# Kernel tuning notes

Hardware: AMD Instinct MI355X
Metric: run time of the kernel (lower is better)

The kernel has to match this reference:

```python
import jax, jax.numpy as jnp
import numpy as np

EPS = 1e-6

def _rms_norm(x, w):
    # per-head RMSNorm over last dim (head_dim)
    var = jnp.mean(jnp.square(x), axis=-1, keepdims=True)
    return x * jax.lax.rsqrt(var + EPS) * w

def _linear(x, w, b):
    # torch nn.Linear: y = x @ W^T + b
    return jnp.einsum('bsd,od->bso', x, w) + b

def setup_inputs() -> dict:
    key = jax.random.key(0)
    ks = jax.random.split(key, 16)
    B, S, S_enc, D, H, HD = 1, 2048, 256, 1536, 24, 64
    w = lambda k: jax.random.normal(k, (D, D), dtype=jnp.float32) * 0.02
    return {
        'hidden_states': jax.random.normal(ks[0], (B, S, D), dtype=jnp.float32),
        'encoder_hidden_states': jax.random.normal(ks[1], (B, S_enc, D), dtype=jnp.float32),
        'attention_mask': jnp.zeros((B, 1, 1, S + S_enc), dtype=jnp.float32),
        'to_q_weight': w(ks[2]), 'to_q_bias': jnp.zeros((D,), jnp.float32),
        'to_k_weight': w(ks[3]), 'to_k_bias': jnp.zeros((D,), jnp.float32),
        'to_v_weight': w(ks[4]), 'to_v_bias': jnp.zeros((D,), jnp.float32),
        'norm_q_weight': jnp.ones((HD,), jnp.float32),
        'norm_k_weight': jnp.ones((HD,), jnp.float32),
        'add_q_proj_weight': w(ks[5]), 'add_q_proj_bias': jnp.zeros((D,), jnp.float32),
        'add_k_proj_weight': w(ks[6]), 'add_k_proj_bias': jnp.zeros((D,), jnp.float32),
        'add_v_proj_weight': w(ks[7]), 'add_v_proj_bias': jnp.zeros((D,), jnp.float32),
        'norm_added_q_weight': jnp.ones((HD,), jnp.float32),
        'norm_added_k_weight': jnp.ones((HD,), jnp.float32),
        'to_out_0_weight': w(ks[8]), 'to_out_0_bias': jnp.zeros((D,), jnp.float32),
        'to_add_out_weight': w(ks[9]), 'to_add_out_bias': jnp.zeros((D,), jnp.float32),
        'attn_heads': 24,
        'attn_head_dim': 64,
    }

def reference(hidden_states, encoder_hidden_states, attention_mask,
              to_q_weight, to_q_bias, to_k_weight, to_k_bias, to_v_weight, to_v_bias,
              norm_q_weight, norm_k_weight,
              add_q_proj_weight, add_q_proj_bias, add_k_proj_weight, add_k_proj_bias,
              add_v_proj_weight, add_v_proj_bias,
              norm_added_q_weight, norm_added_k_weight,
              to_out_0_weight, to_out_0_bias, to_add_out_weight, to_add_out_bias,
              attn_heads, attn_head_dim):
    B, S, D = hidden_states.shape
    S_enc = encoder_hidden_states.shape[1]
    H, HD = attn_heads, attn_head_dim
    scale = float(HD) ** -0.5

    def split_heads(x):  # [B,T,H*HD] -> [B,H,T,HD]
        return x.reshape(B, -1, H, HD).transpose(0, 2, 1, 3)

    # hidden-stream QKV + per-head RMSNorm on q,k
    q = _rms_norm(split_heads(_linear(hidden_states, to_q_weight, to_q_bias)), norm_q_weight)
    k = _rms_norm(split_heads(_linear(hidden_states, to_k_weight, to_k_bias)), norm_k_weight)
    v = split_heads(_linear(hidden_states, to_v_weight, to_v_bias))

    # encoder-stream QKV + per-head RMSNorm on q,k
    eq = _rms_norm(split_heads(_linear(encoder_hidden_states, add_q_proj_weight, add_q_proj_bias)), norm_added_q_weight)
    ek = _rms_norm(split_heads(_linear(encoder_hidden_states, add_k_proj_weight, add_k_proj_bias)), norm_added_k_weight)
    ev = split_heads(_linear(encoder_hidden_states, add_v_proj_weight, add_v_proj_bias))

    # concat streams along sequence: [B,H,S+S_enc,HD]
    q = jnp.concatenate([q, eq], axis=2)
    k = jnp.concatenate([k, ek], axis=2)
    v = jnp.concatenate([v, ev], axis=2)

    # SDPA with additive mask
    scores = jnp.einsum('bhqd,bhkd->bhqk', q, k) * scale + attention_mask
    probs = jax.nn.softmax(scores, axis=-1)
    out = jnp.einsum('bhqk,bhkd->bhqd', probs, v)  # [B,H,T,HD]
    out = out.transpose(0, 2, 1, 3).reshape(B, S + S_enc, H * HD)

    # split back into image / text streams, separate output projections
    attn_output = _linear(out[:, :S], to_out_0_weight, to_out_0_bias)
    context_attn_output = _linear(out[:, S:], to_add_out_weight, to_add_out_bias)
    del context_attn_output  # AttentionFunc returns only the hidden-stream output
    return attn_output
```

## Files before the change

### kernel.cpp

```cpp
#include <hip/hip_runtime.h>
#include <cstdint>


typedef __attribute__((ext_vector_type(8))) short s16x8;
typedef __attribute__((ext_vector_type(4))) float f32x4;

#define LOG2E 1.4426950408889634f

__device__ __forceinline__ short f2bf(float f) {
  union { float f; uint32_t u; } v; v.f = f;
  uint32_t r = v.u + 0x7FFFu + ((v.u >> 16) & 1u);
  return (short)(r >> 16);
}

__device__ __forceinline__ uint32_t cvt_pk_bf16(float lo, float hi) {
  uint32_t r;
  asm("v_cvt_pk_bf16_f32 %0, %1, %2" : "=v"(r) : "v"(lo), "v"(hi));
  return r;
}

typedef uint32_t __attribute__((address_space(1)))* gas_u32;
typedef uint32_t __attribute__((address_space(3)))* las_u32;

__device__ __forceinline__ void gload_lds16(const short* g, short* l) {
  __builtin_amdgcn_global_load_lds((gas_u32)(g), (las_u32)(l), 16, 0, 0);
}

struct CvtSeg { const float* src; short* dst; int n4; };
struct CvtArgs { CvtSeg s[8]; const float* msrc; float* mdst; int mn4; };

__global__ __launch_bounds__(256) void cvt_bf16_kernel(CvtArgs a) {
  const int stride = gridDim.x * blockDim.x;
  const int tid = blockIdx.x * blockDim.x + threadIdx.x;
  for (int i = 0; i < 8; ++i) {
    const float4* src = (const float4*)a.s[i].src;
    short* dst = a.s[i].dst;
    const int n4 = a.s[i].n4;
    for (int j = tid; j < n4; j += stride) {
      float4 v = src[j];
      short4 o;
      o.x = f2bf(v.x); o.y = f2bf(v.y); o.z = f2bf(v.z); o.w = f2bf(v.w);
      *(short4*)(dst + (size_t)j * 4) = o;
    }
  }
  const float4* ms = (const float4*)a.msrc;
  float4* md = (float4*)a.mdst;
  for (int j = tid; j < a.mn4; j += stride) {
    float4 m = ms[j];
    float4 o = {m.x * LOG2E, m.y * LOG2E, m.z * LOG2E, m.w * LOG2E};
    md[j] = o;
  }
}

enum { MODE_Q = 0, MODE_K = 1, MODE_V = 2, MODE_OUT = 3 };

struct GemmCfg {
  const short* A;
  const short* W;
  const float* bias;
  const float* normw;
  void* dst;
  int toff;
  int mode;
  int pad;
};
struct GemmArgs { GemmCfg c[5]; };

__global__ __launch_bounds__(256) void proj_gemm_kernel(GemmArgs args, int chunk) {
  const int w = (blockIdx.x & 7) * chunk + (blockIdx.x >> 3);
  int z, tx, ty;
  if (w < 576) { z = w / 192; const int r = w % 192; tx = r >> 4; ty = r & 15; }
  else { int r = w - 576; z = 3 + r / 24; r %= 24; tx = r >> 1; ty = r & 1; }
  const GemmCfg cfg = args.c[z];
  constexpr int K = 1536;
  __shared__ short As[4096];
  __shared__ short Bs[4096];
  const int t = threadIdx.x;
  const int lane = t & 63;
  const int wave = t >> 6;
  const int l16 = lane & 15;
  const int quad = lane >> 4;
  const int wm = wave >> 1;
  const int wn = wave & 1;

  const short* __restrict__ Ag = cfg.A + (size_t)(ty * 128) * K;
  const short* __restrict__ Wg = cfg.W + (size_t)(tx * 128) * K;
  const int srow = t >> 2;
  const int ssw = ((t & 3) ^ ((srow >> 1) & 3)) << 3;
  const int rsw = (quad ^ ((l16 >> 1) & 3)) << 3;

  const f32x4 z4 = {0.f, 0.f, 0.f, 0.f};
  f32x4 acc[4][4];
#pragma unroll
  for (int i = 0; i < 4; ++i) {
#pragma unroll
    for (int j = 0; j < 4; ++j) acc[i][j] = z4;
  }

  for (int k0 = 0; k0 < K; k0 += 32) {
    gload_lds16(Ag + (size_t)srow * K + k0 + ssw, As + t * 8);
    gload_lds16(Ag + (size_t)(srow + 64) * K + k0 + ssw, As + 2048 + t * 8);
    gload_lds16(Wg + (size_t)srow * K + k0 + ssw, Bs + t * 8);
    gload_lds16(Wg + (size_t)(srow + 64) * K + k0 + ssw, Bs + 2048 + t * 8);
    __syncthreads();
    s16x8 af[4], bfr[4];
#pragma unroll
    for (int i = 0; i < 4; ++i)
      af[i] = *(const s16x8*)(As + (wm * 64 + i * 16 + l16) * 32 + rsw);
#pragma unroll
    for (int i = 0; i < 4; ++i)
      bfr[i] = *(const s16x8*)(Bs + (wn * 64 + i * 16 + l16) * 32 + rsw);
#pragma unroll
    for (int mi = 0; mi < 4; ++mi) {
#pragma unroll
      for (int ni = 0; ni < 4; ++ni)
        acc[mi][ni] = __builtin_amdgcn_mfma_f32_16x16x32_bf16(af[mi], bfr[ni], acc[mi][ni], 0, 0, 0);
    }
    __syncthreads();
  }

  const int nbase = tx * 128 + wn * 64;
  const int mbase = ty * 128 + wm * 64;
  const int mode = cfg.mode;
  const int h = nbase >> 6;

  float biasv[4], nwv[4];
#pragma unroll
  for (int ni = 0; ni < 4; ++ni) {
    int col = nbase + ni * 16 + l16;
    biasv[ni] = cfg.bias[col];
    nwv[ni] = (mode == MODE_Q || mode == MODE_K) ? cfg.normw[col & 63] : 0.f;
  }

#pragma unroll
  for (int mi = 0; mi < 4; ++mi) {
    float vv[4][4];
#pragma unroll
    for (int ni = 0; ni < 4; ++ni) {
#pragma unroll
      for (int r = 0; r < 4; ++r) vv[ni][r] = acc[mi][ni][r] + biasv[ni];
    }
    if (mode == MODE_Q || mode == MODE_K) {
      float ss[4];
#pragma unroll
      for (int r = 0; r < 4; ++r)
        ss[r] = vv[0][r] * vv[0][r] + vv[1][r] * vv[1][r] +
                vv[2][r] * vv[2][r] + vv[3][r] * vv[3][r];
#pragma unroll
      for (int r = 0; r < 4; ++r) {
        ss[r] += __shfl_xor(ss[r], 1);
        ss[r] += __shfl_xor(ss[r], 2);
        ss[r] += __shfl_xor(ss[r], 4);
        ss[r] += __shfl_xor(ss[r], 8);
        float rs = rsqrtf(ss[r] * (1.0f / 64.0f) + 1e-6f);
#pragma unroll
        for (int ni = 0; ni < 4; ++ni) vv[ni][r] *= rs * nwv[ni];
      }
    }
    const int row0 = mbase + mi * 16 + quad * 4;
    if (mode == MODE_Q) {
      short* Qd = (short*)cfg.dst;
#pragma unroll
      for (int ni = 0; ni < 4; ++ni) {
        int d = ni * 16 + l16;
#pragma unroll
        for (int r = 0; r < 4; ++r)
          Qd[((size_t)h * 2048 + row0 + r) * 64 + d] = f2bf(vv[ni][r]);
      }
    } else if (mode == MODE_K) {
      short* Kd = (short*)cfg.dst;
#pragma unroll
      for (int ni = 0; ni < 4; ++ni) {
        int d = ni * 16 + l16;
#pragma unroll
        for (int r = 0; r < 4; ++r)
          Kd[((size_t)h * 2304 + cfg.toff + row0 + r) * 64 + d] = f2bf(vv[ni][r]);
      }
    } else if (mode == MODE_V) {
      short* Vd = (short*)cfg.dst;
#pragma unroll
      for (int ni = 0; ni < 4; ++ni) {
        int d = ni * 16 + l16;
        short4 o4;
        o4.x = f2bf(vv[ni][0]); o4.y = f2bf(vv[ni][1]);
        o4.z = f2bf(vv[ni][2]); o4.w = f2bf(vv[ni][3]);
        *(short4*)(Vd + ((size_t)h * 64 + d) * 2304 + cfg.toff + row0) = o4;
      }
    } else {
      float* Od = (float*)cfg.dst;
#pragma unroll
      for (int ni = 0; ni < 4; ++ni) {
        int col = nbase + ni * 16 + l16;
#pragma unroll
        for (int r = 0; r < 4; ++r)
          Od[(size_t)(row0 + r) * 1536 + col] = vv[ni][r];
      }
    }
  }
}

__global__ __launch_bounds__(256) void flash_kernel(
    const short* __restrict__ Q, const short* __restrict__ Kc,
    const short* __restrict__ VT, const float* __restrict__ mlt,
    short* __restrict__ AO) {
  const int b = blockIdx.x;
  const int h = (b & 7) * 3 + ((b >> 3) % 3);
  const int q0 = ((b >> 3) / 3) * 64;
  const int lane = threadIdx.x & 63;
  const int wave = threadIdx.x >> 6;
  const int qw = wave & 1;
  const int ks = wave >> 1;
  const int l16 = lane & 15;
  const int quad = lane >> 4;

  __shared__ __align__(16) short smem[16384];

  const short* Kh = Kc + (size_t)h * 2304 * 64;
  const short* Vh = VT + (size_t)h * 64 * 2304;

  s16x8 aq0[2], aq1[2];
#pragma unroll
  for (int g = 0; g < 2; ++g) {
    const short* Qrow =
        Q + ((size_t)h * 2048 + q0 + qw * 32 + g * 16 + l16) * 64;
    aq0[g] = *(const s16x8*)(Qrow + quad * 8);
    aq1[g] = *(const s16x8*)(Qrow + quad * 8 + 32);
  }

  s16x8 ones;
#pragma unroll
  for (int i = 0; i < 8; ++i) ones[i] = (short)0x3F80;

  const f32x4 z4 = {0.f, 0.f, 0.f, 0.f};
  f32x4 o[2][4];
#pragma unroll
  for (int g = 0; g < 2; ++g)
#pragma unroll
    for (int mi = 0; mi < 4; ++mi) o[g][mi] = z4;
  f32x4 lacc[2] = {z4, z4};
  const float SC = 0.125f * LOG2E;
  const int kbase = ks * 1152;

  const int gi0 = qw * 64 + lane;
  const int trow0 = gi0 >> 3, cp0 = gi0 & 7;
  const int srow0 = ((trow0 & 12) << 1) | (trow0 & 3);
  const int d0 = gi0 >> 2, cpv0 = gi0 & 3;
  const short* kS = Kh + (size_t)kbase * 64 + srow0 * 64 + ((cp0 ^ (trow0 & 7)) << 3);
  const short* vS = Vh + (size_t)d0 * 2304 + kbase + ((cpv0 ^ ((d0 >> 1) & 3)) << 3);
  const int ldst = qw * 512 + lane * 8;

  auto stage = [&](int it, int buf) {
    short* kt = smem + (ks * 2 + buf) * 2048;
    short* vt = smem + 8192 + (ks * 2 + buf) * 2048;
    const short* ksrc = kS + it * 2048;
    const short* vsrc = vS + it * 32;
    gload_lds16(ksrc,             kt + ldst);
    gload_lds16(ksrc + 256,       kt + 1024 + ldst);
    gload_lds16(vsrc,             vt + ldst);
    gload_lds16(vsrc + 32 * 2304, vt + 1024 + ldst);
  };

  stage(0, 0);
  __syncthreads();

#pragma unroll 2
  for (int it = 0; it < 36; ++it) {
    const int buf = it & 1;
    if (it < 35) stage(it + 1, buf ^ 1);
    const short* kt = smem + (ks * 2 + buf) * 2048;
    const short* vt = smem + 8192 + (ks * 2 + buf) * 2048;
    const int kb = kbase + it * 32;

    s16x8 bk[2][2];
#pragma unroll
    for (int ni = 0; ni < 2; ++ni) {
      const int tt = ni * 16 + l16;
      const short* kr = kt + tt * 64;
      bk[ni][0] = *(const s16x8*)(kr + ((quad ^ (tt & 7)) << 3));
      bk[ni][1] = *(const s16x8*)(kr + (((quad + 4) ^ (tt & 7)) << 3));
    }
    s16x8 bv[4];
#pragma unroll
    for (int mi = 0; mi < 4; ++mi) {
      const int d = mi * 16 + l16;
      bv[mi] = *(const s16x8*)(vt + d * 32 + ((quad ^ ((d >> 1) & 3)) << 3));
    }
    float4 mv0 = *(const float4*)(mlt + kb + quad * 8);
    float4 mv1 = *(const float4*)(mlt + kb + quad * 8 + 4);
    const float m8[8] = {mv0.x, mv0.y, mv0.z, mv0.w, mv1.x, mv1.y, mv1.z, mv1.w};

#pragma unroll
    for (int g = 0; g < 2; ++g) {
      union { uint32_t w[4]; s16x8 v; } pu;
#pragma unroll
      for (int ni = 0; ni < 2; ++ni) {
        f32x4 s = __builtin_amdgcn_mfma_f32_16x16x32_bf16(bk[ni][0], aq0[g], z4, 0, 0, 0);
        s = __builtin_amdgcn_mfma_f32_16x16x32_bf16(bk[ni][1], aq1[g], s, 0, 0, 0);
        float p[4];
#pragma unroll
        for (int rr = 0; rr < 4; ++rr)
          p[rr] = __builtin_amdgcn_exp2f(fmaf(s[rr], SC, m8[ni * 4 + rr]));
        pu.w[ni * 2 + 0] = cvt_pk_bf16(p[0], p[1]);
        pu.w[ni * 2 + 1] = cvt_pk_bf16(p[2], p[3]);
      }
      lacc[g] = __builtin_amdgcn_mfma_f32_16x16x32_bf16(pu.v, ones, lacc[g], 0, 0, 0);
#pragma unroll
      for (int mi = 0; mi < 4; ++mi)
        o[g][mi] = __builtin_amdgcn_mfma_f32_16x16x32_bf16(pu.v, bv[mi], o[g][mi], 0, 0, 0);
    }
    __syncthreads();
  }

  f32x4* R = (f32x4*)smem;
  if (ks == 1) {
    f32x4* Rw = R + (qw * 64 + lane) * 10;
#pragma unroll
    for (int g = 0; g < 2; ++g) {
#pragma unroll
      for (int mi = 0; mi < 4; ++mi) Rw[g * 5 + mi] = o[g][mi];
      Rw[g * 5 + 4] = lacc[g];
    }
  }
  __syncthreads();
  if (ks == 0) {
    const f32x4* Rw = R + (qw * 64 + lane) * 10;
#pragma unroll
    for (int g = 0; g < 2; ++g) {
#pragma unroll
      for (int mi = 0; mi < 4; ++mi) o[g][mi] += Rw[g * 5 + mi];
      f32x4 lt = lacc[g] + Rw[g * 5 + 4];
#pragma unroll
      for (int rr = 0; rr < 4; ++rr) {
        float inv = 1.0f / lt[rr];
        int tq = q0 + qw * 32 + g * 16 + quad * 4 + rr;
#pragma unroll
        for (int mi = 0; mi < 4; ++mi)
          AO[(size_t)tq * 1536 + h * 64 + mi * 16 + l16] = f2bf(o[g][mi][rr] * inv);
      }
    }
  }
}

extern "C" void kernel_launch(void* const* d_in, const int* in_sizes, int n_in,
                              void* d_out, int out_size, void* d_ws, size_t ws_size,
                              hipStream_t stream) {
  (void)in_sizes; (void)n_in; (void)out_size; (void)ws_size;
  const float* hidden = (const float*)d_in[0];
  const float* enc    = (const float*)d_in[1];
  const float* amask  = (const float*)d_in[2];
  const float* wq  = (const float*)d_in[3];  const float* bq  = (const float*)d_in[4];
  const float* wk  = (const float*)d_in[5];  const float* bk  = (const float*)d_in[6];
  const float* wv  = (const float*)d_in[7];  const float* bv  = (const float*)d_in[8];
  const float* nqw = (const float*)d_in[9];  const float* nkw = (const float*)d_in[10];
  const float* wak = (const float*)d_in[13]; const float* bak = (const float*)d_in[14];
  const float* wav = (const float*)d_in[15]; const float* bav = (const float*)d_in[16];
  const float* nakw = (const float*)d_in[18];
  const float* wo  = (const float*)d_in[19]; const float* bo  = (const float*)d_in[20];
  float* out = (float*)d_out;

  char* p = (char*)d_ws;
  auto carve = [&](size_t bytes) { char* r = p; p += (bytes + 255) & ~(size_t)255; return r; };
  short* Xb   = (short*)carve((size_t)2048 * 1536 * 2);
  short* Eb   = (short*)carve((size_t)256 * 1536 * 2);
  short* Wqb  = (short*)carve((size_t)1536 * 1536 * 2);
  short* Wkb  = (short*)carve((size_t)1536 * 1536 * 2);
  short* Wvb  = (short*)carve((size_t)1536 * 1536 * 2);
  short* Wakb = (short*)carve((size_t)1536 * 1536 * 2);
  short* Wavb = (short*)carve((size_t)1536 * 1536 * 2);
  short* Wob  = (short*)carve((size_t)1536 * 1536 * 2);
  short* Qb   = (short*)carve((size_t)24 * 2048 * 64 * 2);
  short* Kb   = (short*)carve((size_t)24 * 2304 * 64 * 2);
  short* VTb  = (short*)carve((size_t)24 * 64 * 2304 * 2);
  short* AOb  = (short*)carve((size_t)2048 * 1536 * 2);
  float* MLb  = (float*)carve((size_t)2304 * 4);

  CvtArgs ca;
  ca.s[0] = {hidden, Xb, 2048 * 1536 / 4};
  ca.s[1] = {enc,    Eb, 256 * 1536 / 4};
  ca.s[2] = {wq,  Wqb,  1536 * 1536 / 4};
  ca.s[3] = {wk,  Wkb,  1536 * 1536 / 4};
  ca.s[4] = {wv,  Wvb,  1536 * 1536 / 4};
  ca.s[5] = {wak, Wakb, 1536 * 1536 / 4};
  ca.s[6] = {wav, Wavb, 1536 * 1536 / 4};
  ca.s[7] = {wo,  Wob,  1536 * 1536 / 4};
  ca.msrc = amask; ca.mdst = MLb; ca.mn4 = 2304 / 4;
  cvt_bf16_kernel<<<dim3(1024), dim3(256), 0, stream>>>(ca);

  GemmArgs g1;
  g1.c[0] = {Xb, Wqb,  bq,  nqw,     (void*)Qb,  0,    MODE_Q, 0};
  g1.c[1] = {Xb, Wkb,  bk,  nkw,     (void*)Kb,  0,    MODE_K, 0};
  g1.c[2] = {Xb, Wvb,  bv,  nullptr, (void*)VTb, 0,    MODE_V, 0};
  g1.c[3] = {Eb, Wakb, bak, nakw,    (void*)Kb,  2048, MODE_K, 0};
  g1.c[4] = {Eb, Wavb, bav, nullptr, (void*)VTb, 2048, MODE_V, 0};
  proj_gemm_kernel<<<dim3(624), dim3(256), 0, stream>>>(g1, 78);

  flash_kernel<<<dim3(768), dim3(256), 0, stream>>>(Qb, Kb, VTb, MLb, AOb);

  GemmArgs g3;
  g3.c[0] = {AOb, Wob, bo, nullptr, (void*)out, 0, MODE_OUT, 0};
  proj_gemm_kernel<<<dim3(192), dim3(256), 0, stream>>>(g3, 24);
}
```

Baseline: 273.5 us.

## Fuse Q/K/V projections into one GEMM kernel sharing the activation tile

Adds a dedicated QKV GEMM kernel where each block loads one 128-row activation tile once and multiplies it against the Q, K and V weight tiles (64 columns each) at the same time, keeping three accumulator sets. The encoder stream does the same with its K and V weights. This cuts activation reloads and the block count from 624 to 432. In exchange each block uses more registers and LDS, which may lower occupancy, and 432 blocks may fill the GPU's compute units less evenly.

Result: no change. 278.9 us (+2.0%).

```diff
diff --git a/kernel.cpp b/kernel.cpp
--- a/kernel.cpp
+++ b/kernel.cpp
@@ -65,6 +65,145 @@
   int pad;
 };
 struct GemmArgs { GemmCfg c[5]; };
+
+__global__ __launch_bounds__(256) void qkv_gemm_kernel(GemmArgs args) {
+  const int w = (blockIdx.x & 7) * 54 + (blockIdx.x >> 3);
+  int zc, tx, ty;
+  GemmCfg s0, s1, s2;
+  if (w < 384) {
+    zc = 3; tx = w >> 4; ty = w & 15;
+    s0 = args.c[0]; s1 = args.c[1]; s2 = args.c[2];
+  } else {
+    const int r = w - 384;
+    zc = 2; tx = r >> 1; ty = r & 1;
+    s0 = args.c[3]; s1 = args.c[4]; s2 = args.c[4];
+  }
+  constexpr int K = 1536;
+  __shared__ short As[4096];
+  __shared__ short Ws[3][2048];
+  const int t = threadIdx.x;
+  const int lane = t & 63;
+  const int wave = t >> 6;
+  const int l16 = lane & 15;
+  const int quad = lane >> 4;
+
+  const short* __restrict__ Ag = s0.A + (size_t)(ty * 128) * K;
+  const short* __restrict__ W0 = s0.W + (size_t)(tx * 64) * K;
+  const short* __restrict__ W1 = s1.W + (size_t)(tx * 64) * K;
+  const short* __restrict__ W2 = s2.W + (size_t)(tx * 64) * K;
+  const int srow = t >> 2;
+  const int ssw = ((t & 3) ^ ((srow >> 1) & 3)) << 3;
+  const int rsw = (quad ^ ((l16 >> 1) & 3)) << 3;
+
+  const f32x4 z4 = {0.f, 0.f, 0.f, 0.f};
+  f32x4 acc[3][2][4];
+#pragma unroll
+  for (int z = 0; z < 3; ++z)
+#pragma unroll
+    for (int i = 0; i < 2; ++i)
+#pragma unroll
+      for (int j = 0; j < 4; ++j) acc[z][i][j] = z4;
+
+  for (int k0 = 0; k0 < K; k0 += 32) {
+    gload_lds16(Ag + (size_t)srow * K + k0 + ssw, As + t * 8);
+    gload_lds16(Ag + (size_t)(srow + 64) * K + k0 + ssw, As + 2048 + t * 8);
+    gload_lds16(W0 + (size_t)srow * K + k0 + ssw, Ws[0] + t * 8);
+    gload_lds16(W1 + (size_t)srow * K + k0 + ssw, Ws[1] + t * 8);
+    if (zc == 3) gload_lds16(W2 + (size_t)srow * K + k0 + ssw, Ws[2] + t * 8);
+    __syncthreads();
+    s16x8 af[2];
+    af[0] = *(const s16x8*)(As + (wave * 32 + l16) * 32 + rsw);
+    af[1] = *(const s16x8*)(As + (wave * 32 + 16 + l16) * 32 + rsw);
+#pragma unroll
+    for (int z = 0; z < 3; ++z) {
+      if (z < zc) {
+        s16x8 bfr[4];
+#pragma unroll
+        for (int i = 0; i < 4; ++i)
+          bfr[i] = *(const s16x8*)(Ws[z] + (i * 16 + l16) * 32 + rsw);
+#pragma unroll
+        for (int mi = 0; mi < 2; ++mi)
+#pragma unroll
+          for (int ni = 0; ni < 4; ++ni)
+            acc[z][mi][ni] = __builtin_amdgcn_mfma_f32_16x16x32_bf16(
+                af[mi], bfr[ni], acc[z][mi][ni], 0, 0, 0);
+      }
+    }
+    __syncthreads();
+  }
+
+  const int h = tx;
+  const int nbase = tx * 64;
+#pragma unroll
+  for (int z = 0; z < 3; ++z) {
+    if (z >= zc) continue;
+    const GemmCfg cfg = (z == 0) ? s0 : (z == 1) ? s1 : s2;
+    const int mode = cfg.mode;
+    float biasv[4], nwv[4];
+#pragma unroll
+    for (int ni = 0; ni < 4; ++ni) {
+      int col = nbase + ni * 16 + l16;
+      biasv[ni] = cfg.bias[col];
+      nwv[ni] = (mode == MODE_Q || mode == MODE_K) ? cfg.normw[col & 63] : 0.f;
+    }
+#pragma unroll
+    for (int mi = 0; mi < 2; ++mi) {
+      float vv[4][4];
+#pragma unroll
+      for (int ni = 0; ni < 4; ++ni) {
+#pragma unroll
+        for (int r = 0; r < 4; ++r) vv[ni][r] = acc[z][mi][ni][r] + biasv[ni];
+      }
+      if (mode == MODE_Q || mode == MODE_K) {
+        float ss[4];
+#pragma unroll
+        for (int r = 0; r < 4; ++r)
+          ss[r] = vv[0][r] * vv[0][r] + vv[1][r] * vv[1][r] +
+                  vv[2][r] * vv[2][r] + vv[3][r] * vv[3][r];
+#pragma unroll
+        for (int r = 0; r < 4; ++r) {
+          ss[r] += __shfl_xor(ss[r], 1);
+          ss[r] += __shfl_xor(ss[r], 2);
+          ss[r] += __shfl_xor(ss[r], 4);
+          ss[r] += __shfl_xor(ss[r], 8);
+          float rs = rsqrtf(ss[r] * (1.0f / 64.0f) + 1e-6f);
+#pragma unroll
+          for (int ni = 0; ni < 4; ++ni) vv[ni][r] *= rs * nwv[ni];
+        }
+      }
+      const int row0 = ty * 128 + wave * 32 + mi * 16 + quad * 4;
+      if (mode == MODE_Q) {
+        short* Qd = (short*)cfg.dst;
+#pragma unroll
+        for (int ni = 0; ni < 4; ++ni) {
+          int d = ni * 16 + l16;
+#pragma unroll
+          for (int r = 0; r < 4; ++r)
+            Qd[((size_t)h * 2048 + row0 + r) * 64 + d] = f2bf(vv[ni][r]);
+        }
+      } else if (mode == MODE_K) {
+        short* Kd = (short*)cfg.dst;
+#pragma unroll
+        for (int ni = 0; ni < 4; ++ni) {
+          int d = ni * 16 + l16;
+#pragma unroll
+          for (int r = 0; r < 4; ++r)
+            Kd[((size_t)h * 2304 + cfg.toff + row0 + r) * 64 + d] = f2bf(vv[ni][r]);
+        }
+      } else {
+        short* Vd = (short*)cfg.dst;
+#pragma unroll
+        for (int ni = 0; ni < 4; ++ni) {
+          int d = ni * 16 + l16;
+          short4 o4;
+          o4.x = f2bf(vv[ni][0]); o4.y = f2bf(vv[ni][1]);
+          o4.z = f2bf(vv[ni][2]); o4.w = f2bf(vv[ni][3]);
+          *(short4*)(Vd + ((size_t)h * 64 + d) * 2304 + cfg.toff + row0) = o4;
+        }
+      }
+    }
+  }
+}
 
 __global__ __launch_bounds__(256) void proj_gemm_kernel(GemmArgs args, int chunk) {
   const int w = (blockIdx.x & 7) * chunk + (blockIdx.x >> 3);
@@ -392,7 +531,7 @@
   g1.c[2] = {Xb, Wvb,  bv,  nullptr, (void*)VTb, 0,    MODE_V, 0};
   g1.c[3] = {Eb, Wakb, bak, nakw,    (void*)Kb,  2048, MODE_K, 0};
   g1.c[4] = {Eb, Wavb, bav, nullptr, (void*)VTb, 2048, MODE_V, 0};
-  proj_gemm_kernel<<<dim3(624), dim3(256), 0, stream>>>(g1, 78);
+  qkv_gemm_kernel<<<dim3(432), dim3(256), 0, stream>>>(g1);
 
   flash_kernel<<<dim3(768), dim3(256), 0, stream>>>(Qb, Kb, VTb, MLb, AOb);
 
```

## Fuse fp32-to-bf16 weight conversion into projection GEMM tile loads

Applied to the files above, without the earlier changes.

The separate pass that converted the six 1536x1536 fp32 weight matrices to bf16 is removed. The GEMM now streams fp32 weights straight into LDS through a new XOR-swizzled layout and converts them to bf16 in registers before the MFMAs. This drops a full read and write of the weights in the conversion kernel and the bf16 reread. In exchange, each weight tile is converted redundantly by every M-tile block, and weight global loads and LDS use double.

Result: slower. 333.4 us (+21.9%).

```diff
diff --git a/kernel.cpp b/kernel.cpp
--- a/kernel.cpp
+++ b/kernel.cpp
@@ -22,17 +22,17 @@
 typedef uint32_t __attribute__((address_space(1)))* gas_u32;
 typedef uint32_t __attribute__((address_space(3)))* las_u32;
 
-__device__ __forceinline__ void gload_lds16(const short* g, short* l) {
+__device__ __forceinline__ void gload_lds16(const void* g, void* l) {
   __builtin_amdgcn_global_load_lds((gas_u32)(g), (las_u32)(l), 16, 0, 0);
 }
 
 struct CvtSeg { const float* src; short* dst; int n4; };
-struct CvtArgs { CvtSeg s[8]; const float* msrc; float* mdst; int mn4; };
+struct CvtArgs { CvtSeg s[2]; const float* msrc; float* mdst; int mn4; };
 
 __global__ __launch_bounds__(256) void cvt_bf16_kernel(CvtArgs a) {
   const int stride = gridDim.x * blockDim.x;
   const int tid = blockIdx.x * blockDim.x + threadIdx.x;
-  for (int i = 0; i < 8; ++i) {
+  for (int i = 0; i < 2; ++i) {
     const float4* src = (const float4*)a.s[i].src;
     short* dst = a.s[i].dst;
     const int n4 = a.s[i].n4;
@@ -56,7 +56,7 @@
 
 struct GemmCfg {
   const short* A;
-  const short* W;
+  const float* W;
   const float* bias;
   const float* normw;
   void* dst;
@@ -74,7 +74,7 @@
   const GemmCfg cfg = args.c[z];
   constexpr int K = 1536;
   __shared__ short As[4096];
-  __shared__ short Bs[4096];
+  __shared__ float Bsf[4096];
   const int t = threadIdx.x;
   const int lane = t & 63;
   const int wave = t >> 6;
@@ -84,10 +84,14 @@
   const int wn = wave & 1;
 
   const short* __restrict__ Ag = cfg.A + (size_t)(ty * 128) * K;
-  const short* __restrict__ Wg = cfg.W + (size_t)(tx * 128) * K;
+  const float* __restrict__ Wg = cfg.W + (size_t)(tx * 128) * K;
   const int srow = t >> 2;
   const int ssw = ((t & 3) ^ ((srow >> 1) & 3)) << 3;
   const int rsw = (quad ^ ((l16 >> 1) & 3)) << 3;
+  const int wrow = t >> 3;
+  const int wsw = ((t & 7) ^ (wrow & 7)) << 2;
+  const int wc0 = ((2 * quad) ^ (l16 & 7)) << 2;
+  const int wc1 = ((2 * quad + 1) ^ (l16 & 7)) << 2;
 
   const f32x4 z4 = {0.f, 0.f, 0.f, 0.f};
   f32x4 acc[4][4];
@@ -100,16 +104,25 @@
   for (int k0 = 0; k0 < K; k0 += 32) {
     gload_lds16(Ag + (size_t)srow * K + k0 + ssw, As + t * 8);
     gload_lds16(Ag + (size_t)(srow + 64) * K + k0 + ssw, As + 2048 + t * 8);
-    gload_lds16(Wg + (size_t)srow * K + k0 + ssw, Bs + t * 8);
-    gload_lds16(Wg + (size_t)(srow + 64) * K + k0 + ssw, Bs + 2048 + t * 8);
+#pragma unroll
+    for (int j = 0; j < 4; ++j)
+      gload_lds16(Wg + (size_t)(wrow + j * 32) * K + k0 + wsw,
+                  Bsf + ((size_t)j * 256 + t) * 4);
     __syncthreads();
     s16x8 af[4], bfr[4];
 #pragma unroll
     for (int i = 0; i < 4; ++i)
       af[i] = *(const s16x8*)(As + (wm * 64 + i * 16 + l16) * 32 + rsw);
 #pragma unroll
-    for (int i = 0; i < 4; ++i)
-      bfr[i] = *(const s16x8*)(Bs + (wn * 64 + i * 16 + l16) * 32 + rsw);
+    for (int i = 0; i < 4; ++i) {
+      const float* wr = Bsf + (wn * 64 + i * 16 + l16) * 32;
+      float4 f0 = *(const float4*)(wr + wc0);
+      float4 f1 = *(const float4*)(wr + wc1);
+      s16x8 b;
+      b[0] = f2bf(f0.x); b[1] = f2bf(f0.y); b[2] = f2bf(f0.z); b[3] = f2bf(f0.w);
+      b[4] = f2bf(f1.x); b[5] = f2bf(f1.y); b[6] = f2bf(f1.z); b[7] = f2bf(f1.w);
+      bfr[i] = b;
+    }
 #pragma unroll
     for (int mi = 0; mi < 4; ++mi) {
 #pragma unroll
@@ -362,12 +375,6 @@
   auto carve = [&](size_t bytes) { char* r = p; p += (bytes + 255) & ~(size_t)255; return r; };
   short* Xb   = (short*)carve((size_t)2048 * 1536 * 2);
   short* Eb   = (short*)carve((size_t)256 * 1536 * 2);
-  short* Wqb  = (short*)carve((size_t)1536 * 1536 * 2);
-  short* Wkb  = (short*)carve((size_t)1536 * 1536 * 2);
-  short* Wvb  = (short*)carve((size_t)1536 * 1536 * 2);
-  short* Wakb = (short*)carve((size_t)1536 * 1536 * 2);
-  short* Wavb = (short*)carve((size_t)1536 * 1536 * 2);
-  short* Wob  = (short*)carve((size_t)1536 * 1536 * 2);
   short* Qb   = (short*)carve((size_t)24 * 2048 * 64 * 2);
   short* Kb   = (short*)carve((size_t)24 * 2304 * 64 * 2);
   short* VTb  = (short*)carve((size_t)24 * 64 * 2304 * 2);
@@ -377,26 +384,20 @@
   CvtArgs ca;
   ca.s[0] = {hidden, Xb, 2048 * 1536 / 4};
   ca.s[1] = {enc,    Eb, 256 * 1536 / 4};
-  ca.s[2] = {wq,  Wqb,  1536 * 1536 / 4};
-  ca.s[3] = {wk,  Wkb,  1536 * 1536 / 4};
-  ca.s[4] = {wv,  Wvb,  1536 * 1536 / 4};
-  ca.s[5] = {wak, Wakb, 1536 * 1536 / 4};
-  ca.s[6] = {wav, Wavb, 1536 * 1536 / 4};
-  ca.s[7] = {wo,  Wob,  1536 * 1536 / 4};
   ca.msrc = amask; ca.mdst = MLb; ca.mn4 = 2304 / 4;
   cvt_bf16_kernel<<<dim3(1024), dim3(256), 0, stream>>>(ca);
 
   GemmArgs g1;
-  g1.c[0] = {Xb, Wqb,  bq,  nqw,     (void*)Qb,  0,    MODE_Q, 0};
-  g1.c[1] = {Xb, Wkb,  bk,  nkw,     (void*)Kb,  0,    MODE_K, 0};
-  g1.c[2] = {Xb, Wvb,  bv,  nullptr, (void*)VTb, 0,    MODE_V, 0};
-  g1.c[3] = {Eb, Wakb, bak, nakw,    (void*)Kb,  2048, MODE_K, 0};
-  g1.c[4] = {Eb, Wavb, bav, nullptr, (void*)VTb, 2048, MODE_V, 0};
+  g1.c[0] = {Xb, wq,  bq,  nqw,     (void*)Qb,  0,    MODE_Q, 0};
+  g1.c[1] = {Xb, wk,  bk,  nkw,     (void*)Kb,  0,    MODE_K, 0};
+  g1.c[2] = {Xb, wv,  bv,  nullptr, (void*)VTb, 0,    MODE_V, 0};
+  g1.c[3] = {Eb, wak, bak, nakw,    (void*)Kb,  2048, MODE_K, 0};
+  g1.c[4] = {Eb, wav, bav, nullptr, (void*)VTb, 2048, MODE_V, 0};
   proj_gemm_kernel<<<dim3(624), dim3(256), 0, stream>>>(g1, 78);
 
   flash_kernel<<<dim3(768), dim3(256), 0, stream>>>(Qb, Kb, VTb, MLb, AOb);
 
   GemmArgs g3;
-  g3.c[0] = {AOb, Wob, bo, nullptr, (void*)out, 0, MODE_OUT, 0};
+  g3.c[0] = {AOb, wo, bo, nullptr, (void*)out, 0, MODE_OUT, 0};
   proj_gemm_kernel<<<dim3(192), dim3(256), 0, stream>>>(g3, 24);
 }
```
